# Performance work log

Measured on AMD Instinct MI355X. Metric: run time of the kernel, lower is better.

Reference implementation:

```python
import jax, jax.numpy as jnp
import numpy as np
import math

H = 12
DH = 64
MAX_POS = 1024

def setup_inputs() -> dict:
    key = jax.random.key(0)
    ks = jax.random.split(key, 8)
    B, L, D = 2, 1024, 768
    s = 0.02
    return {
        "hidden_states": jax.random.normal(ks[0], (B, L, D), jnp.float32),
        "attention_mask": jnp.zeros((B, 1, 1, L), jnp.float32),
        "struct_matrix": jax.random.uniform(ks[1], (5, B, 1, L, L), jnp.float32),
        "Wq": jax.random.normal(ks[2], (D, D), jnp.float32) * s,
        "bq": jnp.zeros((D,), jnp.float32),
        "Wk": jax.random.normal(ks[3], (D, D), jnp.float32) * s,
        "bk": jnp.zeros((D,), jnp.float32),
        "Wv": jax.random.normal(ks[4], (D, D), jnp.float32) * s,
        "bv": jnp.zeros((D,), jnp.float32),
        "dist_emb": jax.random.normal(ks[5], (2 * MAX_POS - 1, DH), jnp.float32) * s,
        "ssan_w": jax.random.normal(ks[6], (5, H, DH, DH), jnp.float32) * s,
        "abs_bias": jnp.zeros((5, H), jnp.float32),
    }

def reference(hidden_states, attention_mask, struct_matrix, Wq, bq, Wk, bk, Wv, bv, dist_emb, ssan_w, abs_bias):
    B, L, D = hidden_states.shape

    def heads(x):  # [B,L,D] -> [B,H,L,dh]
        return x.reshape(B, L, H, DH).transpose(0, 2, 1, 3)

    q = heads(hidden_states @ Wq + bq)
    k = heads(hidden_states @ Wk + bk)
    v = heads(hidden_states @ Wv + bv)

    scores = jnp.einsum('bhqd,bhkd->bhqk', q, k)

    # relative_key_query positional scores
    pos_ids = jnp.arange(L)
    distance = pos_ids[:, None] - pos_ids[None, :]          # [L,L]
    pos = dist_emb[distance + MAX_POS - 1]                  # [L,L,dh]
    scores = scores + jnp.einsum('bhld,lrd->bhlr', q, pos)
    scores = scores + jnp.einsum('bhrd,lrd->bhlr', k, pos)

    scores = scores / math.sqrt(DH)
    scores = scores + attention_mask

    # 5 SSAN bilinear bias terms, masked by structural matrices
    for i in range(5):
        bias = jnp.einsum('bhqd,hde,bhke->bhqk', q, ssan_w[i], k)
        scores = scores + (bias + abs_bias[i][None, :, None, None]) * struct_matrix[i]

    probs = jax.nn.softmax(scores, axis=-1)
    ctx = jnp.einsum('bhqk,bhkd->bqhd', probs, v).reshape(B, L, D)
    return ctx
```

## Files before the change

kernel.cpp:

```cpp
#include <hip/hip_runtime.h>
#include <math.h>

#define NB 2
#define NL 1024
#define ND 768
#define NH 12
#define DH 64

typedef _Float16 f16;
typedef _Float16 f16x4 __attribute__((ext_vector_type(4)));
typedef _Float16 f16x8 __attribute__((ext_vector_type(8)));
typedef float f32x4 __attribute__((ext_vector_type(4)));

#define MFMA16(a, b, c) __builtin_amdgcn_mfma_f32_16x16x32_f16((a), (b), (c), 0, 0, 0)

__global__ __launch_bounds__(256) void prep_kernel(
    const float* __restrict__ hs,
    const float* __restrict__ Wq, const float* __restrict__ Wk,
    const float* __restrict__ Wv, const float* __restrict__ sw,
    f16* __restrict__ hsf, f16* __restrict__ wt, f16* __restrict__ swt)
{
    __shared__ float sT[64 * 66];
    const int t = threadIdx.x;
    const int tile = blockIdx.x;

    if (tile < 768) {
        const int base = tile * 2048 + t * 8;
        float4 a = *(const float4*)&hs[base];
        float4 b = *(const float4*)&hs[base + 4];
        f16x8 hv;
        hv[0] = (f16)a.x; hv[1] = (f16)a.y; hv[2] = (f16)a.z; hv[3] = (f16)a.w;
        hv[4] = (f16)b.x; hv[5] = (f16)b.y; hv[6] = (f16)b.z; hv[7] = (f16)b.w;
        *(f16x8*)&hsf[base] = hv;
        return;
    }

    const float* S; f16* D; int sRS, dRS;
    const int ti = tile - 768;
    if (ti < 432) {
        const int mat = ti / 144, r2 = ti % 144, ht = r2 / 12, kt = r2 % 12;
        const float* W = (mat == 0) ? Wq : (mat == 1) ? Wk : Wv;
        S = W + (size_t)(kt * 64) * ND + ht * 64;
        D = wt + (size_t)((mat * NH + ht) * 64) * ND + kt * 64;
        sRS = ND; dRS = ND;
    } else {
        const int i = ti - 432;
        S = sw + (size_t)i * 4096;
        D = swt + (size_t)i * 4096;
        sRS = 64; dRS = 64;
    }

    {
        const int kk = t >> 2, nb = (t & 3) * 16;
        float v[16];
        #pragma unroll
        for (int j = 0; j < 4; ++j)
            *(float4*)&v[4 * j] = *(const float4*)&S[(size_t)kk * sRS + nb + 4 * j];
        #pragma unroll
        for (int jj = 0; jj < 16; ++jj)
            sT[(nb + jj) * 66 + kk] = v[jj];
    }
    __syncthreads();
    {
        const int n = t >> 2, kb = (t & 3) * 16;
        f16 tmp[16];
        #pragma unroll
        for (int j = 0; j < 8; ++j) {
            float2 x = *(float2*)&sT[n * 66 + kb + 2 * j];
            tmp[2 * j]     = (f16)x.x;
            tmp[2 * j + 1] = (f16)x.y;
        }
        *(f16x8*)&D[(size_t)n * dRS + kb]     = *(f16x8*)&tmp[0];
        *(f16x8*)&D[(size_t)n * dRS + kb + 8] = *(f16x8*)&tmp[8];
    }
}

__global__ __launch_bounds__(256, 4) void qkv_kernel(
    const f16* __restrict__ hsf, const f16* __restrict__ wt,
    const float* __restrict__ bq, const float* __restrict__ bk,
    const float* __restrict__ bv,
    f16* __restrict__ qf, f16* __restrict__ kf, f16* __restrict__ vt)
{
    __shared__ f16 sA[64 * 72], sB[64 * 72];
    __shared__ float sT[64 * 66];

    const int m0  = blockIdx.x * 64;
    const int y   = blockIdx.y;
    const int mat = y / NH, h = y % NH;
    const int t = threadIdx.x, lane = t & 63, w = t >> 6;
    const int quad = lane >> 4, l15 = lane & 15;
    const int wm = w >> 1, wn = w & 1;

    const float* bias = (mat == 0) ? bq : (mat == 1) ? bk : bv;

    f32x4 acc[2][2];
    #pragma unroll
    for (int r = 0; r < 2; ++r)
        #pragma unroll
        for (int c = 0; c < 2; ++c) acc[r][c] = (f32x4){0.f, 0.f, 0.f, 0.f};

    const int srow = t >> 2, scol = (t & 3) * 16;
    const f16* Ag = hsf + (size_t)(m0 + srow) * ND + scol;
    const f16* Bg = wt + ((size_t)y * 64 + srow) * ND + scol;

    for (int k0 = 0; k0 < ND; k0 += 64) {
        __syncthreads();
        *(f16x8*)&sA[srow * 72 + scol]     = *(const f16x8*)&Ag[k0];
        *(f16x8*)&sA[srow * 72 + scol + 8] = *(const f16x8*)&Ag[k0 + 8];
        *(f16x8*)&sB[srow * 72 + scol]     = *(const f16x8*)&Bg[k0];
        *(f16x8*)&sB[srow * 72 + scol + 8] = *(const f16x8*)&Bg[k0 + 8];
        __syncthreads();
        #pragma unroll
        for (int kk = 0; kk < 64; kk += 32) {
            const int ko = kk + quad * 8;
            f16x8 a0 = *(f16x8*)&sA[(32 * wm + l15) * 72 + ko];
            f16x8 a1 = *(f16x8*)&sA[(32 * wm + 16 + l15) * 72 + ko];
            f16x8 b0 = *(f16x8*)&sB[(32 * wn + l15) * 72 + ko];
            f16x8 b1 = *(f16x8*)&sB[(32 * wn + 16 + l15) * 72 + ko];
            acc[0][0] = MFMA16(a0, b0, acc[0][0]);
            acc[0][1] = MFMA16(a0, b1, acc[0][1]);
            acc[1][0] = MFMA16(a1, b0, acc[1][0]);
            acc[1][1] = MFMA16(a1, b1, acc[1][1]);
        }
    }
    __syncthreads();

    const int bb = m0 >> 10;
    const int lbase = m0 & 1023;
    const int bh = bb * NH + h;

    if (mat < 2) {
        #pragma unroll
        for (int r = 0; r < 2; ++r)
            #pragma unroll
            for (int c = 0; c < 2; ++c) {
                const int col = 32 * wn + 16 * c + l15;
                const float bz = bias[h * 64 + col];
                #pragma unroll
                for (int rr = 0; rr < 4; ++rr)
                    sT[(32 * wm + 16 * r + 4 * quad + rr) * 66 + col] = acc[r][c][rr] + bz;
            }
        __syncthreads();
        const int orow = t >> 2, ocb = (t & 3) * 16;
        f16 tmp[16];
        #pragma unroll
        for (int j = 0; j < 8; ++j) {
            float2 x = *(float2*)&sT[orow * 66 + ocb + 2 * j];
            tmp[2 * j] = (f16)x.x; tmp[2 * j + 1] = (f16)x.y;
        }
        f16* dst = ((mat == 0) ? qf : kf) + ((size_t)bh * NL + lbase + orow) * DH + ocb;
        *(f16x8*)dst       = *(f16x8*)&tmp[0];
        *(f16x8*)(dst + 8) = *(f16x8*)&tmp[8];
    } else {
        #pragma unroll
        for (int r = 0; r < 2; ++r)
            #pragma unroll
            for (int c = 0; c < 2; ++c) {
                const int col = 32 * wn + 16 * c + l15;
                const float bz = bias[h * 64 + col];
                #pragma unroll
                for (int rr = 0; rr < 4; ++rr)
                    sT[col * 66 + 32 * wm + 16 * r + 4 * quad + rr] = acc[r][c][rr] + bz;
            }
        __syncthreads();
        const int d = t >> 2, lcb = (t & 3) * 16;
        f16 tmp[16];
        #pragma unroll
        for (int j = 0; j < 8; ++j) {
            float2 x = *(float2*)&sT[d * 66 + lcb + 2 * j];
            tmp[2 * j] = (f16)x.x; tmp[2 * j + 1] = (f16)x.y;
        }
        f16* dst = vt + ((size_t)bh * DH + d) * NL + lbase + lcb;
        *(f16x8*)dst       = *(f16x8*)&tmp[0];
        *(f16x8*)(dst + 8) = *(f16x8*)&tmp[8];
    }
}

__global__ __launch_bounds__(256, 4) void qw_kernel(
    const f16* __restrict__ qf, const f16* __restrict__ swt,
    f16* __restrict__ qwf)
{
    __shared__ f16 sA[64 * 72], sB[64 * 72];
    __shared__ float sT[64 * 66];

    const int l0 = blockIdx.x * 64;
    const int z  = blockIdx.y;
    const int p  = z / 24, bh = z % 24, h = bh % NH;
    const int t = threadIdx.x, lane = t & 63, w = t >> 6;
    const int quad = lane >> 4, l15 = lane & 15;
    const int wm = w >> 1, wn = w & 1;

    const int srow = t >> 2, scol = (t & 3) * 16;
    {
        const f16* As = qf + ((size_t)bh * NL + l0 + srow) * DH + scol;
        const f16* Bs = swt + ((size_t)(p * NH + h) * 64 + srow) * 64 + scol;
        *(f16x8*)&sA[srow * 72 + scol]     = *(const f16x8*)As;
        *(f16x8*)&sA[srow * 72 + scol + 8] = *(const f16x8*)(As + 8);
        *(f16x8*)&sB[srow * 72 + scol]     = *(const f16x8*)Bs;
        *(f16x8*)&sB[srow * 72 + scol + 8] = *(const f16x8*)(Bs + 8);
    }
    __syncthreads();

    f32x4 acc[2][2];
    #pragma unroll
    for (int r = 0; r < 2; ++r)
        #pragma unroll
        for (int c = 0; c < 2; ++c) acc[r][c] = (f32x4){0.f, 0.f, 0.f, 0.f};

    #pragma unroll
    for (int kk = 0; kk < 64; kk += 32) {
        const int ko = kk + quad * 8;
        f16x8 a0 = *(f16x8*)&sA[(32 * wm + l15) * 72 + ko];
        f16x8 a1 = *(f16x8*)&sA[(32 * wm + 16 + l15) * 72 + ko];
        f16x8 b0 = *(f16x8*)&sB[(32 * wn + l15) * 72 + ko];
        f16x8 b1 = *(f16x8*)&sB[(32 * wn + 16 + l15) * 72 + ko];
        acc[0][0] = MFMA16(a0, b0, acc[0][0]);
        acc[0][1] = MFMA16(a0, b1, acc[0][1]);
        acc[1][0] = MFMA16(a1, b0, acc[1][0]);
        acc[1][1] = MFMA16(a1, b1, acc[1][1]);
    }
    __syncthreads();

    #pragma unroll
    for (int r = 0; r < 2; ++r)
        #pragma unroll
        for (int c = 0; c < 2; ++c) {
            const int col = 32 * wn + 16 * c + l15;
            #pragma unroll
            for (int rr = 0; rr < 4; ++rr)
                sT[(32 * wm + 16 * r + 4 * quad + rr) * 66 + col] = acc[r][c][rr];
        }
    __syncthreads();

    const int orow = t >> 2, ocb = (t & 3) * 16;
    f16 tmp[16];
    #pragma unroll
    for (int j = 0; j < 8; ++j) {
        float2 x = *(float2*)&sT[orow * 66 + ocb + 2 * j];
        tmp[2 * j] = (f16)x.x; tmp[2 * j + 1] = (f16)x.y;
    }
    f16* dst = qwf + ((size_t)(p * 24 + bh) * NL + l0 + orow) * DH + ocb;
    *(f16x8*)dst       = *(f16x8*)&tmp[0];
    *(f16x8*)(dst + 8) = *(f16x8*)&tmp[8];
}

__global__ __launch_bounds__(256, 2) void pos_kernel(
    const f16* __restrict__ qf, const f16* __restrict__ kf,
    const float* __restrict__ dist_emb, f16* __restrict__ posb)
{
    __shared__ f16 sQ[64 * 72], sK2[64 * 72];
    __shared__ f16 sE[128 * 72];
    __shared__ f16 sQE[64 * 140], sKE[64 * 140];

    const int l0 = blockIdx.x * 64;
    const int r0 = blockIdx.y * 64;
    const int bh = blockIdx.z;
    const int t  = threadIdx.x;
    const int lane = t & 63;
    const int w    = t >> 6;
    const int quad = lane >> 4;
    const int l15  = lane & 15;

    {
        const int row = t >> 3, col = (t & 7) * 8;
        const f16* qs = qf + ((size_t)bh * NL + l0) * DH;
        const f16* ks = kf + ((size_t)bh * NL + r0) * DH;
        *(f16x8*)&sQ[row * 72 + col]        = *(const f16x8*)&qs[row * 64 + col];
        *(f16x8*)&sQ[(row + 32) * 72 + col] = *(const f16x8*)&qs[(row + 32) * 64 + col];
        *(f16x8*)&sK2[row * 72 + col]        = *(const f16x8*)&ks[row * 64 + col];
        *(f16x8*)&sK2[(row + 32) * 72 + col] = *(const f16x8*)&ks[(row + 32) * 64 + col];
        const int ebase = l0 - r0 + 960;
        #pragma unroll
        for (int p = 0; p < 4; ++p) {
            const int er = row + 32 * p;
            if (er < 127) {
                const float* es = dist_emb + (size_t)(ebase + er) * DH + col;
                float4 a = *(const float4*)es;
                float4 b = *(const float4*)(es + 4);
                f16x8 hv;
                hv[0] = (f16)a.x; hv[1] = (f16)a.y; hv[2] = (f16)a.z; hv[3] = (f16)a.w;
                hv[4] = (f16)b.x; hv[5] = (f16)b.y; hv[6] = (f16)b.z; hv[7] = (f16)b.w;
                *(f16x8*)&sE[er * 72 + col] = hv;
            }
        }
    }
    __syncthreads();

    {
        const int arow = (16 * w + l15) * 72 + quad * 8;
        f16x8 aq0 = *(f16x8*)&sQ[arow];
        f16x8 aq1 = *(f16x8*)&sQ[arow + 32];
        f16x8 ak0 = *(f16x8*)&sK2[arow];
        f16x8 ak1 = *(f16x8*)&sK2[arow + 32];
        #pragma unroll
        for (int n = 0; n < 8; ++n) {
            const int brow = (16 * n + l15) * 72 + quad * 8;
            f16x8 e0 = *(f16x8*)&sE[brow];
            f16x8 e1 = *(f16x8*)&sE[brow + 32];
            f32x4 cq = {0.f, 0.f, 0.f, 0.f};
            cq = MFMA16(aq0, e0, cq);
            cq = MFMA16(aq1, e1, cq);
            f32x4 ck = {0.f, 0.f, 0.f, 0.f};
            ck = MFMA16(ak0, e0, ck);
            ck = MFMA16(ak1, e1, ck);
            #pragma unroll
            for (int r = 0; r < 4; ++r) {
                sQE[(16 * w + 4 * quad + r) * 140 + 16 * n + l15] = (f16)cq[r];
                sKE[(16 * w + 4 * quad + r) * 140 + 16 * n + l15] = (f16)ck[r];
            }
        }
    }
    __syncthreads();

    {
        const int i  = t >> 2;
        const int j0 = (t & 3) * 16;
        f16 res[16];
        #pragma unroll
        for (int jj = 0; jj < 16; ++jj) {
            const int j = j0 + jj;
            const int tt = i - j + 63;
            float v = (float)sQE[i * 140 + tt] + (float)sKE[j * 140 + tt];
            res[jj] = (f16)v;
        }
        f16* dst = posb + ((size_t)bh * NL + l0 + i) * NL + r0 + j0;
        *(f16x8*)dst       = *(f16x8*)&res[0];
        *(f16x8*)(dst + 8) = *(f16x8*)&res[8];
    }
}

__global__ __launch_bounds__(256, 2) void attn_kernel(
    const f16* __restrict__ qf, const f16* __restrict__ kf,
    const f16* __restrict__ vt, const f16* __restrict__ qwf,
    const float* __restrict__ mask, const float* __restrict__ struct_m,
    const f16* __restrict__ posb, const float* __restrict__ abs_bias,
    float* __restrict__ out)
{
    __shared__ f16 sK[64 * 72];
    __shared__ f16 sVt[2][64 * 72];
    __shared__ float sS[32 * 68];
    __shared__ f16 sP[32 * 72];
    __shared__ float sAlpha[32], sL[32];

    const int l0 = blockIdx.x * 32;
    const int bh = blockIdx.y;
    const int bb = bh / NH, h = bh % NH;
    const int t  = threadIdx.x;
    const int lane  = t & 63;
    const int w     = t >> 6;
    const int quad  = lane >> 4;
    const int l15   = lane & 15;
    const int msub  = w >> 1;
    const int npair = w & 1;

    const size_t NQKV = (size_t)NB * NH * NL * DH;

    f16x8 aQ[2], aW[5][2];
    {
        const size_t qrow = ((size_t)bh * NL + l0 + 16 * msub + l15) * DH;
        #pragma unroll
        for (int K = 0; K < 2; ++K) {
            aQ[K] = *(const f16x8*)&qf[qrow + 32 * K + 8 * quad];
            #pragma unroll
            for (int p = 0; p < 5; ++p)
                aW[p][K] = *(const f16x8*)&qwf[p * NQKV + qrow + 32 * K + 8 * quad];
        }
    }

    float ab[5];
    #pragma unroll
    for (int p = 0; p < 5; ++p) ab[p] = abs_bias[p * NH + h];

    float pf_st[5][2][4], pf_pos[2][4], pf_mask[2];

    auto stage_kv = [&](int r0s, int buf) {
        const int row = t >> 3, col = (t & 7) * 8;
        const f16* ks = kf + ((size_t)bh * NL + r0s) * DH;
        *(f16x8*)&sK[row * 72 + col]        = *(const f16x8*)&ks[row * 64 + col];
        *(f16x8*)&sK[(row + 32) * 72 + col] = *(const f16x8*)&ks[(row + 32) * 64 + col];
        const f16* vs = vt + (size_t)bh * DH * NL + r0s;
        *(f16x8*)&sVt[buf][row * 72 + col] =
            *(const f16x8*)&vs[(size_t)row * NL + col];
        *(f16x8*)&sVt[buf][(row + 32) * 72 + col] =
            *(const f16x8*)&vs[(size_t)(row + 32) * NL + col];
    };

    auto prefetch = [&](int r0s) {
        #pragma unroll
        for (int n = 0; n < 2; ++n) {
            const int j = 32 * npair + 16 * n + l15;
            pf_mask[n] = mask[bb * NL + r0s + j];
            #pragma unroll
            for (int r = 0; r < 4; ++r) {
                const int i = 16 * msub + 4 * quad + r;
                pf_pos[n][r] = (float)posb[((size_t)bh * NL + l0 + i) * NL + r0s + j];
                #pragma unroll
                for (int p = 0; p < 5; ++p)
                    pf_st[p][n][r] =
                        struct_m[((size_t)(p * NB + bb) * NL + l0 + i) * NL + r0s + j];
            }
        }
    };

    stage_kv(0, 0);
    prefetch(0);

    const int sm_i = t >> 3;
    const int sm_jb = t & 7;
    float m_cur = -INFINITY, l_cur = 0.f;
    f32x4 O[2];
    O[0] = (f32x4){0.f, 0.f, 0.f, 0.f};
    O[1] = (f32x4){0.f, 0.f, 0.f, 0.f};

    for (int kt = 0; kt < 16; ++kt) {
        const int cur = kt & 1;
        __syncthreads();

        {
            f32x4 acc[2][6];
            #pragma unroll
            for (int n = 0; n < 2; ++n)
                #pragma unroll
                for (int p = 0; p < 6; ++p)
                    acc[n][p] = (f32x4){0.f, 0.f, 0.f, 0.f};

            #pragma unroll
            for (int K = 0; K < 2; ++K) {
                const int koff = K * 32 + quad * 8;
                f16x8 bk2[2];
                #pragma unroll
                for (int n = 0; n < 2; ++n)
                    bk2[n] = *(f16x8*)&sK[(32 * npair + 16 * n + l15) * 72 + koff];
                #pragma unroll
                for (int n = 0; n < 2; ++n)
                    acc[n][0] = MFMA16(aQ[K], bk2[n], acc[n][0]);
                #pragma unroll
                for (int p = 0; p < 5; ++p)
                    #pragma unroll
                    for (int n = 0; n < 2; ++n)
                        acc[n][1 + p] = MFMA16(aW[p][K], bk2[n], acc[n][1 + p]);
            }

            #pragma unroll
            for (int n = 0; n < 2; ++n) {
                const int j = 32 * npair + 16 * n + l15;
                #pragma unroll
                for (int r = 0; r < 4; ++r) {
                    const int i = 16 * msub + 4 * quad + r;
                    float s = (acc[n][0][r] + pf_pos[n][r]) * 0.125f + pf_mask[n];
                    #pragma unroll
                    for (int p = 0; p < 5; ++p)
                        s += (acc[n][1 + p][r] + ab[p]) * pf_st[p][n][r];
                    sS[i * 68 + j] = s;
                }
            }
        }
        __syncthreads();

        {
            float sv[8];
            float smax = -INFINITY;
            #pragma unroll
            for (int k = 0; k < 8; ++k) {
                sv[k] = sS[sm_i * 68 + sm_jb + 8 * k];
                smax = fmaxf(smax, sv[k]);
            }
            #pragma unroll
            for (int off = 4; off > 0; off >>= 1)
                smax = fmaxf(smax, __shfl_xor(smax, off, 8));
            const float m_new = fmaxf(m_cur, smax);
            const float alpha = __expf(m_cur - m_new);
            float rsum = 0.f;
            #pragma unroll
            for (int k = 0; k < 8; ++k) {
                float p = __expf(sv[k] - m_new);
                sP[sm_i * 72 + sm_jb + 8 * k] = (f16)p;
                rsum += p;
            }
            #pragma unroll
            for (int off = 4; off > 0; off >>= 1)
                rsum += __shfl_xor(rsum, off, 8);
            l_cur = l_cur * alpha + rsum;
            m_cur = m_new;
            if (sm_jb == 0) { sAlpha[sm_i] = alpha; sL[sm_i] = l_cur; }
        }
        __syncthreads();

        {
            float a4[4];
            #pragma unroll
            for (int r = 0; r < 4; ++r) a4[r] = sAlpha[16 * msub + 4 * quad + r];
            #pragma unroll
            for (int n = 0; n < 2; ++n)
                #pragma unroll
                for (int r = 0; r < 4; ++r) O[n][r] *= a4[r];

            const int prow = (16 * msub + l15) * 72;
            #pragma unroll
            for (int K = 0; K < 2; ++K) {
                const int koff = K * 32 + quad * 8;
                f16x8 pfr = *(f16x8*)&sP[prow + koff];
                #pragma unroll
                for (int n = 0; n < 2; ++n) {
                    f16x8 vfr = *(f16x8*)&sVt[cur][(32 * npair + 16 * n + l15) * 72 + koff];
                    O[n] = MFMA16(pfr, vfr, O[n]);
                }
            }

            if (kt < 15) {
                stage_kv((kt + 1) * 64, cur ^ 1);
                prefetch((kt + 1) * 64);
            }
        }
    }

    float linv[4];
    #pragma unroll
    for (int r = 0; r < 4; ++r) linv[r] = 1.0f / sL[16 * msub + 4 * quad + r];
    #pragma unroll
    for (int n = 0; n < 2; ++n) {
        const int dh = 32 * npair + 16 * n + l15;
        #pragma unroll
        for (int r = 0; r < 4; ++r) {
            const int i = 16 * msub + 4 * quad + r;
            out[((size_t)bb * NL + l0 + i) * ND + h * DH + dh] = O[n][r] * linv[r];
        }
    }
}

extern "C" void kernel_launch(void* const* d_in, const int* in_sizes, int n_in,
                              void* d_out, int out_size, void* d_ws, size_t ws_size,
                              hipStream_t stream) {
    const float* hs   = (const float*)d_in[0];
    const float* mask = (const float*)d_in[1];
    const float* stm  = (const float*)d_in[2];
    const float* Wq   = (const float*)d_in[3];
    const float* bq   = (const float*)d_in[4];
    const float* Wk   = (const float*)d_in[5];
    const float* bk   = (const float*)d_in[6];
    const float* Wv   = (const float*)d_in[7];
    const float* bv   = (const float*)d_in[8];
    const float* de   = (const float*)d_in[9];
    const float* sw   = (const float*)d_in[10];
    const float* abb  = (const float*)d_in[11];
    float* outp = (float*)d_out;

    const size_t NQKV = (size_t)NB * NH * NL * DH;
    char* ws = (char*)d_ws;
    f16* qf   = (f16*)ws;                 ws += NQKV * 2;
    f16* kf   = (f16*)ws;                 ws += NQKV * 2;
    f16* vtb  = (f16*)ws;                 ws += NQKV * 2;
    f16* qwf  = (f16*)ws;                 ws += 5 * NQKV * 2;
    f16* posb = (f16*)ws;
    f16* hsf = posb;
    f16* wt  = hsf + NQKV;
    f16* swt = wt + (size_t)2304 * 768;

    prep_kernel<<<1260, 256, 0, stream>>>(hs, Wq, Wk, Wv, sw, hsf, wt, swt);
    qkv_kernel<<<dim3(32, 36), 256, 0, stream>>>(hsf, wt, bq, bk, bv, qf, kf, vtb);
    qw_kernel<<<dim3(16, 120), 256, 0, stream>>>(qf, swt, qwf);
    pos_kernel<<<dim3(16, 16, 24), 256, 0, stream>>>(qf, kf, de, posb);
    attn_kernel<<<dim3(32, 24), 256, 0, stream>>>(qf, kf, vtb, qwf,
                                                  mask, stm, posb, abb, outp);
}
```

Before: 247.7 us.

## Use lightweight LDS barriers, pre-convert dist_emb to f16, issue KV staging earlier

Replaces __syncthreads with an inline-asm barrier that waits only on LDS/scalar counters (lgkmcnt), so outstanding global memory operations are not drained at every barrier. Converts dist_emb to f16 once in the prep kernel, so pos_kernel loads half the bytes and skips per-tile conversion. In the attention loop, the next K/V tile staging and prefetch are issued before the PV MFMAs rather than after, to overlap memory latency with compute. The custom barrier relies on the compiler not needing vmcnt waits at those points, which adds correctness risk if any LDS write depends on an unfinished global load.

Result: no change. 246.0 us (-0.7%).

```diff
diff --git a/kernel.cpp b/kernel.cpp
--- a/kernel.cpp
+++ b/kernel.cpp
@@ -14,11 +14,17 @@
 
 #define MFMA16(a, b, c) __builtin_amdgcn_mfma_f32_16x16x32_f16((a), (b), (c), 0, 0, 0)
 
+__device__ __forceinline__ void soft_barrier() {
+    asm volatile("s_waitcnt lgkmcnt(0)\n\ts_barrier" ::: "memory");
+}
+
 __global__ __launch_bounds__(256) void prep_kernel(
     const float* __restrict__ hs,
     const float* __restrict__ Wq, const float* __restrict__ Wk,
     const float* __restrict__ Wv, const float* __restrict__ sw,
-    f16* __restrict__ hsf, f16* __restrict__ wt, f16* __restrict__ swt)
+    const float* __restrict__ de,
+    f16* __restrict__ hsf, f16* __restrict__ wt, f16* __restrict__ swt,
+    f16* __restrict__ de16)
 {
     __shared__ float sT[64 * 66];
     const int t = threadIdx.x;
@@ -32,6 +38,18 @@
         hv[0] = (f16)a.x; hv[1] = (f16)a.y; hv[2] = (f16)a.z; hv[3] = (f16)a.w;
         hv[4] = (f16)b.x; hv[5] = (f16)b.y; hv[6] = (f16)b.z; hv[7] = (f16)b.w;
         *(f16x8*)&hsf[base] = hv;
+        return;
+    }
+    if (tile >= 1260) {
+        const int base = (tile - 1260) * 2048 + t * 8;
+        if (base < 2047 * 64) {
+            float4 a = *(const float4*)&de[base];
+            float4 b = *(const float4*)&de[base + 4];
+            f16x8 hv;
+            hv[0] = (f16)a.x; hv[1] = (f16)a.y; hv[2] = (f16)a.z; hv[3] = (f16)a.w;
+            hv[4] = (f16)b.x; hv[5] = (f16)b.y; hv[6] = (f16)b.z; hv[7] = (f16)b.w;
+            *(f16x8*)&de16[base] = hv;
+        }
         return;
     }
 
@@ -60,7 +78,7 @@
         for (int jj = 0; jj < 16; ++jj)
             sT[(nb + jj) * 66 + kk] = v[jj];
     }
-    __syncthreads();
+    soft_barrier();
     {
         const int n = t >> 2, kb = (t & 3) * 16;
         f16 tmp[16];
@@ -104,12 +122,12 @@
     const f16* Bg = wt + ((size_t)y * 64 + srow) * ND + scol;
 
     for (int k0 = 0; k0 < ND; k0 += 64) {
-        __syncthreads();
+        soft_barrier();
         *(f16x8*)&sA[srow * 72 + scol]     = *(const f16x8*)&Ag[k0];
         *(f16x8*)&sA[srow * 72 + scol + 8] = *(const f16x8*)&Ag[k0 + 8];
         *(f16x8*)&sB[srow * 72 + scol]     = *(const f16x8*)&Bg[k0];
         *(f16x8*)&sB[srow * 72 + scol + 8] = *(const f16x8*)&Bg[k0 + 8];
-        __syncthreads();
+        soft_barrier();
         #pragma unroll
         for (int kk = 0; kk < 64; kk += 32) {
             const int ko = kk + quad * 8;
@@ -123,7 +141,7 @@
             acc[1][1] = MFMA16(a1, b1, acc[1][1]);
         }
     }
-    __syncthreads();
+    soft_barrier();
 
     const int bb = m0 >> 10;
     const int lbase = m0 & 1023;
@@ -140,7 +158,7 @@
                 for (int rr = 0; rr < 4; ++rr)
                     sT[(32 * wm + 16 * r + 4 * quad + rr) * 66 + col] = acc[r][c][rr] + bz;
             }
-        __syncthreads();
+        soft_barrier();
         const int orow = t >> 2, ocb = (t & 3) * 16;
         f16 tmp[16];
         #pragma unroll
@@ -162,7 +180,7 @@
                 for (int rr = 0; rr < 4; ++rr)
                     sT[col * 66 + 32 * wm + 16 * r + 4 * quad + rr] = acc[r][c][rr] + bz;
             }
-        __syncthreads();
+        soft_barrier();
         const int d = t >> 2, lcb = (t & 3) * 16;
         f16 tmp[16];
         #pragma unroll
@@ -199,7 +217,7 @@
         *(f16x8*)&sB[srow * 72 + scol]     = *(const f16x8*)Bs;
         *(f16x8*)&sB[srow * 72 + scol + 8] = *(const f16x8*)(Bs + 8);
     }
-    __syncthreads();
+    soft_barrier();
 
     f32x4 acc[2][2];
     #pragma unroll
@@ -219,7 +237,7 @@
         acc[1][0] = MFMA16(a1, b0, acc[1][0]);
         acc[1][1] = MFMA16(a1, b1, acc[1][1]);
     }
-    __syncthreads();
+    soft_barrier();
 
     #pragma unroll
     for (int r = 0; r < 2; ++r)
@@ -230,7 +248,7 @@
             for (int rr = 0; rr < 4; ++rr)
                 sT[(32 * wm + 16 * r + 4 * quad + rr) * 66 + col] = acc[r][c][rr];
         }
-    __syncthreads();
+    soft_barrier();
 
     const int orow = t >> 2, ocb = (t & 3) * 16;
     f16 tmp[16];
@@ -246,7 +264,7 @@
 
 __global__ __launch_bounds__(256, 2) void pos_kernel(
     const f16* __restrict__ qf, const f16* __restrict__ kf,
-    const float* __restrict__ dist_emb, f16* __restrict__ posb)
+    const f16* __restrict__ de16, f16* __restrict__ posb)
 {
     __shared__ f16 sQ[64 * 72], sK2[64 * 72];
     __shared__ f16 sE[128 * 72];
@@ -273,18 +291,12 @@
         #pragma unroll
         for (int p = 0; p < 4; ++p) {
             const int er = row + 32 * p;
-            if (er < 127) {
-                const float* es = dist_emb + (size_t)(ebase + er) * DH + col;
-                float4 a = *(const float4*)es;
-                float4 b = *(const float4*)(es + 4);
-                f16x8 hv;
-                hv[0] = (f16)a.x; hv[1] = (f16)a.y; hv[2] = (f16)a.z; hv[3] = (f16)a.w;
-                hv[4] = (f16)b.x; hv[5] = (f16)b.y; hv[6] = (f16)b.z; hv[7] = (f16)b.w;
-                *(f16x8*)&sE[er * 72 + col] = hv;
-            }
-        }
-    }
-    __syncthreads();
+            if (er < 127)
+                *(f16x8*)&sE[er * 72 + col] =
+                    *(const f16x8*)&de16[(size_t)(ebase + er) * DH + col];
+        }
+    }
+    soft_barrier();
 
     {
         const int arow = (16 * w + l15) * 72 + quad * 8;
@@ -310,7 +322,7 @@
             }
         }
     }
-    __syncthreads();
+    soft_barrier();
 
     {
         const int i  = t >> 2;
@@ -414,7 +426,7 @@
 
     for (int kt = 0; kt < 16; ++kt) {
         const int cur = kt & 1;
-        __syncthreads();
+        soft_barrier();
 
         {
             f32x4 acc[2][6];
@@ -455,7 +467,7 @@
                 }
             }
         }
-        __syncthreads();
+        soft_barrier();
 
         {
             float sv[8];
@@ -484,9 +496,14 @@
             m_cur = m_new;
             if (sm_jb == 0) { sAlpha[sm_i] = alpha; sL[sm_i] = l_cur; }
         }
-        __syncthreads();
+        soft_barrier();
 
         {
+            if (kt < 15) {
+                stage_kv((kt + 1) * 64, cur ^ 1);
+                prefetch((kt + 1) * 64);
+            }
+
             float a4[4];
             #pragma unroll
             for (int r = 0; r < 4; ++r) a4[r] = sAlpha[16 * msub + 4 * quad + r];
@@ -505,11 +522,6 @@
                     f16x8 vfr = *(f16x8*)&sVt[cur][(32 * npair + 16 * n + l15) * 72 + koff];
                     O[n] = MFMA16(pfr, vfr, O[n]);
                 }
-            }
-
-            if (kt < 15) {
-                stage_kv((kt + 1) * 64, cur ^ 1);
-                prefetch((kt + 1) * 64);
             }
         }
     }
@@ -551,15 +563,17 @@
     f16* kf   = (f16*)ws;                 ws += NQKV * 2;
     f16* vtb  = (f16*)ws;                 ws += NQKV * 2;
     f16* qwf  = (f16*)ws;                 ws += 5 * NQKV * 2;
-    f16* posb = (f16*)ws;
+    f16* posb = (f16*)ws;                 ws += (size_t)24 * 1024 * 1024 * 2;
+    f16* de16 = (f16*)ws;
     f16* hsf = posb;
     f16* wt  = hsf + NQKV;
     f16* swt = wt + (size_t)2304 * 768;
 
-    prep_kernel<<<1260, 256, 0, stream>>>(hs, Wq, Wk, Wv, sw, hsf, wt, swt);
+    prep_kernel<<<1324, 256, 0, stream>>>(hs, Wq, Wk, Wv, sw, de,
+                                          hsf, wt, swt, de16);
     qkv_kernel<<<dim3(32, 36), 256, 0, stream>>>(hsf, wt, bq, bk, bv, qf, kf, vtb);
     qw_kernel<<<dim3(16, 120), 256, 0, stream>>>(qf, swt, qwf);
-    pos_kernel<<<dim3(16, 16, 24), 256, 0, stream>>>(qf, kf, de, posb);
+    pos_kernel<<<dim3(16, 16, 24), 256, 0, stream>>>(qf, kf, de16, posb);
     attn_kernel<<<dim3(32, 24), 256, 0, stream>>>(qf, kf, vtb, qwf,
                                                   mask, stm, posb, abb, outp);
 }
```
